# Performance work log

Measured on AMD Instinct MI355X. Metric: run time of the kernel, lower is better.

Reference implementation:

```python
import jax, jax.numpy as jnp
import numpy as np

D_MODEL = 256
N_HEADS = 4
D_HEAD = D_MODEL // N_HEADS
SCALE = 1.0 / np.sqrt(D_HEAD).astype(np.float32)


def setup_inputs() -> dict:
    key = jax.random.key(0)
    ks = jax.random.split(key, 8)
    B, T, S = 4, 512, 512
    return {
        "query": jax.random.normal(ks[0], (B, T, D_MODEL), dtype=jnp.float32),
        "key": jax.random.normal(ks[1], (B, S, D_MODEL), dtype=jnp.float32),
        "value": jax.random.normal(ks[2], (B, S, D_MODEL), dtype=jnp.float32),
        "w_q": jax.random.normal(ks[3], (D_MODEL, D_MODEL), dtype=jnp.float32) * 0.05,
        "w_k": jax.random.normal(ks[4], (D_MODEL, D_MODEL), dtype=jnp.float32) * 0.05,
        "w_v": jax.random.normal(ks[5], (D_MODEL, D_MODEL), dtype=jnp.float32) * 0.05,
        "v_a": jax.random.normal(ks[6], (N_HEADS, D_HEAD), dtype=jnp.float32),
        "w_o": jax.random.normal(ks[7], (D_MODEL, D_MODEL), dtype=jnp.float32) * 0.05,
    }


def reference(query, key, value, w_q, w_k, w_v, v_a, w_o):
    B, T, _ = query.shape
    S = key.shape[1]
    # projections; weights stored as (out, in) like nn.Linear -> x @ W.T
    Q = (query @ w_q.T).reshape(B, T, N_HEADS, D_HEAD).transpose(0, 2, 1, 3)  # bhtd
    K = (key @ w_k.T).reshape(B, S, N_HEADS, D_HEAD).transpose(0, 2, 1, 3)    # bhsd
    V = (value @ w_v.T).reshape(B, S, N_HEADS, D_HEAD).transpose(0, 2, 1, 3)  # bhsd
    # additive (Bahdanau) scores: tanh broadcast of shape (B,H,T,S,Dh)
    combined = jnp.tanh(Q[:, :, :, None, :] + K[:, :, None, :, :])
    scores = jnp.einsum('bhtsd,hd->bhts', combined, v_a) * SCALE
    attn = jax.nn.softmax(scores, axis=-1)  # (B,H,T,S)
    attended = jnp.einsum('bhts,bhsd->bhtd', attn, V)
    attended = attended.transpose(0, 2, 1, 3).reshape(B, T, D_MODEL)
    out = attended @ w_o.T
    return out, attn
```

## Files before the change

### kernel.cpp

```cpp
#include <hip/hip_runtime.h>
#include <math.h>

#define BATCH 4
#define TLEN 512
#define SLEN 512
#define DM 256
#define NH 4
#define DH 64
#define BT (BATCH * TLEN)

__device__ __forceinline__ float rcp_fast(float x) { return __builtin_amdgcn_rcpf(x); }

__global__ __launch_bounds__(256) void transposeN_kernel(
    const float* __restrict__ s0, const float* __restrict__ s1,
    const float* __restrict__ s2, const float* __restrict__ s3,
    float* __restrict__ d0, float* __restrict__ d1,
    float* __restrict__ d2, float* __restrict__ d3) {
  __shared__ float tile[64][65];
  int m = blockIdx.y;
  const float* S = (m == 0) ? s0 : (m == 1) ? s1 : (m == 2) ? s2 : s3;
  float* D = (m == 0) ? d0 : (m == 1) ? d1 : (m == 2) ? d2 : d3;
  int bx = blockIdx.x;
  int to = (bx & 3) * 64;
  int tk = (bx >> 2) * 64;
  int lo = threadIdx.x >> 6;
  int lk = threadIdx.x & 63;
#pragma unroll
  for (int p = 0; p < 16; ++p) {
    int o = p * 4 + lo;
    tile[o][lk] = S[(size_t)(to + o) * DM + tk + lk];
  }
  __syncthreads();
#pragma unroll
  for (int p = 0; p < 16; ++p) {
    int kk = p * 4 + lo;
    D[(size_t)(tk + kk) * DM + to + lk] = tile[lk][kk];
  }
}

__global__ __launch_bounds__(256) void proj_kernel(
    const float* __restrict__ q, const float* __restrict__ k, const float* __restrict__ v,
    const float* __restrict__ wqt, const float* __restrict__ wkt, const float* __restrict__ wvt,
    float* __restrict__ EQ, float* __restrict__ EKT, float* __restrict__ Vw) {
  int tid = threadIdx.x;
  int lane = tid & 63;
  int wid = __builtin_amdgcn_readfirstlane(tid >> 6);
  int which = blockIdx.y;
  const float* X = (which == 0) ? q : (which == 1) ? k : v;
  const float* WT = (which == 0) ? wqt : (which == 1) ? wkt : wvt;
  int row0 = (blockIdx.x >> 2) * 16 + wid * 4;
  int o = (blockIdx.x & 3) * 64 + lane;
  const float* xb = X + (size_t)row0 * DM;
  const float* wcol = WT + o;
  float a0 = 0.f, a1 = 0.f, a2 = 0.f, a3 = 0.f;
#pragma unroll 8
  for (int kk = 0; kk < DM; ++kk) {
    float w = wcol[(size_t)kk * DM];
    a0 = fmaf(xb[kk], w, a0);
    a1 = fmaf(xb[DM + kk], w, a1);
    a2 = fmaf(xb[2 * DM + kk], w, a2);
    a3 = fmaf(xb[3 * DM + kk], w, a3);
  }
  int h = o >> 6, d = o & 63;
  float accs[4] = {a0, a1, a2, a3};
#pragma unroll
  for (int r = 0; r < 4; ++r) {
    int row = row0 + r;
    int b = row >> 9, t = row & 511;
    int bh = b * NH + h;
    float val = accs[r];
    if (which < 2) {
      val = __expf(2.f * fminf(fmaxf(val, -5.5f), 5.5f));
    }
    if (which == 0) {
      EQ[((size_t)bh * TLEN + t) * DH + d] = val;
    } else if (which == 1) {
      EKT[(((size_t)bh * 16 + (d >> 2)) * SLEN + t) * 4 + (d & 3)] = val;
    } else {
      Vw[(size_t)bh * SLEN * DH + (size_t)(t >> 1) * 128 + d * 2 + (t & 1)] = val;
    }
  }
}

__global__ __launch_bounds__(256, 8) void attn_kernel(
    const float* __restrict__ EQ, const float* __restrict__ EKT,
    const float* __restrict__ Vw, const float* __restrict__ va_g,
    float* __restrict__ attn_out, float* __restrict__ attended) {
  __shared__ float pw[4][SLEN];
  __shared__ float fp[4][4][64];
  __shared__ float sred[4][4];
  int tid = threadIdx.x;
  int lane = tid & 63;
  int wid = __builtin_amdgcn_readfirstlane(tid >> 6);
  int bx = (int)((blockIdx.x & 7) * 256 + (blockIdx.x >> 3));
  int bh = bx >> 7;
  int tile = (bx & 127) * 4;
  int h = bh & 3, b = bh >> 2;
  int sq0 = wid * 128;

  const float4* ekf = (const float4*)EKT + (size_t)bh * (16 * SLEN) + sq0 + lane;
  const float* eqb = EQ + ((size_t)bh * TLEN + tile) * DH;
  const float* vap = va_g + h * DH;

  float acc[4][2];
#pragma unroll
  for (int t = 0; t < 4; ++t) { acc[t][0] = 0.f; acc[t][1] = 0.f; }
  float vsum = 0.f;

  float4 eA0, eA1, eB0, eB1;

#define LOADE(EV, dc_) do { EV##0 = ekf[(size_t)(dc_) * SLEN]; \
                            EV##1 = ekf[(size_t)(dc_) * SLEN + 64]; } while (0)

#define SC4(E, qv, av, aref) do {                                           \
    float A0 = fmaf(qv.x, E.x, 1.f), A1 = fmaf(qv.y, E.y, 1.f);             \
    float A2 = fmaf(qv.z, E.z, 1.f), A3 = fmaf(qv.w, E.w, 1.f);             \
    float n01 = fmaf(av.x, A1, av.y * A0);                                  \
    float n23 = fmaf(av.z, A3, av.w * A2);                                  \
    float P01 = A0 * A1, P23 = A2 * A3;                                     \
    float Nm = fmaf(n01, P23, n23 * P01);                                   \
    aref = fmaf(Nm, rcp_fast(P01 * P23), aref);                             \
  } while (0)

#define DCBODY(CUR, NXT, dc_) do {                                          \
    float4 av = *(const float4*)(vap + (dc_) * 4);                          \
    float4 q0 = *(const float4*)(eqb + 0 * DH + (dc_) * 4);                 \
    float4 q1 = *(const float4*)(eqb + 1 * DH + (dc_) * 4);                 \
    float4 q2 = *(const float4*)(eqb + 2 * DH + (dc_) * 4);                 \
    float4 q3 = *(const float4*)(eqb + 3 * DH + (dc_) * 4);                 \
    vsum += (av.x + av.y) + (av.z + av.w);                                  \
    if ((dc_) < 15) LOADE(NXT, (dc_) + 1);                                  \
    __builtin_amdgcn_sched_barrier(0);                                      \
    SC4(CUR##0, q0, av, acc[0][0]); SC4(CUR##1, q0, av, acc[0][1]);         \
    SC4(CUR##0, q1, av, acc[1][0]); SC4(CUR##1, q1, av, acc[1][1]);         \
    SC4(CUR##0, q2, av, acc[2][0]); SC4(CUR##1, q2, av, acc[2][1]);         \
    SC4(CUR##0, q3, av, acc[3][0]); SC4(CUR##1, q3, av, acc[3][1]);         \
  } while (0)

  LOADE(eA, 0);
#pragma unroll 1
  for (int dc2 = 0; dc2 < 8; ++dc2) {
    DCBODY(eA, eB, 2 * dc2);
    DCBODY(eB, eA, 2 * dc2 + 1);
  }

  size_t bht = (size_t)bh * TLEN + tile;
  float e0[4], e1[4];
#pragma unroll
  for (int t = 0; t < 4; ++t) {
    float x0 = __expf(fmaf(acc[t][0], -0.25f, vsum * 0.125f));
    float x1 = __expf(fmaf(acc[t][1], -0.25f, vsum * 0.125f));
    e0[t] = x0; e1[t] = x1;
    float es = x0 + x1;
#pragma unroll
    for (int off = 32; off; off >>= 1) es += __shfl_xor(es, off);
    if (lane == 0) sred[t][wid] = es;
  }
  __syncthreads();
#pragma unroll
  for (int t = 0; t < 4; ++t) {
    float es = (sred[t][0] + sred[t][1]) + (sred[t][2] + sred[t][3]);
    float inv = rcp_fast(es);
    float p0 = e0[t] * inv, p1 = e1[t] * inv;
    pw[t][sq0 + lane] = p0;
    pw[t][sq0 + 64 + lane] = p1;
    float* arow = attn_out + (bht + t) * SLEN + sq0;
    arow[lane] = p0;
    arow[64 + lane] = p1;
  }

  const float2* vb = (const float2*)Vw + (size_t)bh * (256 * 64) + (size_t)(wid * 64) * 64 + lane;
  float f[4];
#pragma unroll
  for (int t = 0; t < 4; ++t) f[t] = 0.f;
#pragma unroll 2
  for (int i = 0; i < 32; ++i) {
    float2 v01 = vb[(size_t)i * 128];
    float2 v23 = vb[(size_t)i * 128 + 64];
    int sb = sq0 + i * 4;
#pragma unroll
    for (int t = 0; t < 4; ++t) {
      float4 pq = *(const float4*)&pw[t][sb];
      f[t] = fmaf(pq.x, v01.x, f[t]);
      f[t] = fmaf(pq.y, v01.y, f[t]);
      f[t] = fmaf(pq.z, v23.x, f[t]);
      f[t] = fmaf(pq.w, v23.y, f[t]);
    }
  }
#pragma unroll
  for (int t = 0; t < 4; ++t) fp[wid][t][lane] = f[t];
  __syncthreads();
  {
    int t = wid;
    float s = (fp[0][t][lane] + fp[1][t][lane]) + (fp[2][t][lane] + fp[3][t][lane]);
    attended[((size_t)(b * TLEN) + tile + t) * DM + h * DH + lane] = s;
  }
}

__global__ __launch_bounds__(256) void outproj_kernel(
    const float* __restrict__ att, const float* __restrict__ wot,
    float* __restrict__ out) {
  int tid = threadIdx.x;
  int lane = tid & 63;
  int wid = __builtin_amdgcn_readfirstlane(tid >> 6);
  int row0 = (blockIdx.x >> 2) * 16 + wid * 4;
  int o = (blockIdx.x & 3) * 64 + lane;
  const float* xb = att + (size_t)row0 * DM;
  const float* wcol = wot + o;
  float a0 = 0.f, a1 = 0.f, a2 = 0.f, a3 = 0.f;
#pragma unroll 8
  for (int kk = 0; kk < DM; ++kk) {
    float w = wcol[(size_t)kk * DM];
    a0 = fmaf(xb[kk], w, a0);
    a1 = fmaf(xb[DM + kk], w, a1);
    a2 = fmaf(xb[2 * DM + kk], w, a2);
    a3 = fmaf(xb[3 * DM + kk], w, a3);
  }
  out[(size_t)(row0 + 0) * DM + o] = a0;
  out[(size_t)(row0 + 1) * DM + o] = a1;
  out[(size_t)(row0 + 2) * DM + o] = a2;
  out[(size_t)(row0 + 3) * DM + o] = a3;
}

extern "C" void kernel_launch(void* const* d_in, const int* in_sizes, int n_in,
                              void* d_out, int out_size, void* d_ws, size_t ws_size,
                              hipStream_t stream) {
  const float* query = (const float*)d_in[0];
  const float* key   = (const float*)d_in[1];
  const float* value = (const float*)d_in[2];
  const float* wq    = (const float*)d_in[3];
  const float* wk    = (const float*)d_in[4];
  const float* wv    = (const float*)d_in[5];
  const float* va    = (const float*)d_in[6];
  const float* wo    = (const float*)d_in[7];

  float* out  = (float*)d_out;
  float* attn = out + (size_t)BT * DM;

  const size_t SEG = (size_t)BT * DM;
  float* EQ  = (float*)d_ws;
  float* EKT = EQ + SEG;
  float* Vw  = EKT + SEG;
  float* att = Vw + SEG;

  bool big_ws = ws_size >= (4 * SEG + 4 * (size_t)DM * DM) * sizeof(float);

  if (big_ws) {
    float* WTq = att + SEG;
    float* WTk = WTq + (size_t)DM * DM;
    float* WTv = WTk + (size_t)DM * DM;
    float* WoT = WTv + (size_t)DM * DM;
    transposeN_kernel<<<dim3(16, 4), 256, 0, stream>>>(wq, wk, wv, wo, WTq, WTk, WTv, WoT);
    proj_kernel<<<dim3(512, 3), 256, 0, stream>>>(query, key, value, WTq, WTk, WTv, EQ, EKT, Vw);
    attn_kernel<<<dim3(2048), 256, 0, stream>>>(EQ, EKT, Vw, va, attn, att);
    outproj_kernel<<<dim3(512), 256, 0, stream>>>(att, WoT, out);
  } else {
    float* WTq = att;
    float* WTk = att + (size_t)DM * DM;
    float* WTv = att + 2 * (size_t)DM * DM;
    float* WoT = EQ;
    transposeN_kernel<<<dim3(16, 3), 256, 0, stream>>>(wq, wk, wv, wv, WTq, WTk, WTv, WTv);
    proj_kernel<<<dim3(512, 3), 256, 0, stream>>>(query, key, value, WTq, WTk, WTv, EQ, EKT, Vw);
    attn_kernel<<<dim3(2048), 256, 0, stream>>>(EQ, EKT, Vw, va, attn, att);
    transposeN_kernel<<<dim3(16, 1), 256, 0, stream>>>(wo, wo, wo, wo, WoT, WoT, WoT, WoT);
    outproj_kernel<<<dim3(512), 256, 0, stream>>>(att, WoT, out);
  }
}
```

Baseline: 88.71 us.

## Stage weight tiles in LDS and drop separate weight transpose kernel

Removes the transpose kernel launch. The projection and output-projection GEMMs now load untransposed weight rows into padded LDS in two K-halves, and each wave computes 8 rows instead of 4, which halves the grid. This saves one launch and the global transpose round-trip, and raises reuse of each weight value. The cost is extra syncthreads, about 33KB of LDS per block, and fewer blocks, which lowers occupancy and parallelism.

```diff
diff --git a/kernel.cpp b/kernel.cpp
--- a/kernel.cpp
+++ b/kernel.cpp
@@ -8,67 +8,69 @@
 #define NH 4
 #define DH 64
 #define BT (BATCH * TLEN)
+#define WPAD 132
 
 __device__ __forceinline__ float rcp_fast(float x) { return __builtin_amdgcn_rcpf(x); }
 
-__global__ __launch_bounds__(256) void transposeN_kernel(
-    const float* __restrict__ s0, const float* __restrict__ s1,
-    const float* __restrict__ s2, const float* __restrict__ s3,
-    float* __restrict__ d0, float* __restrict__ d1,
-    float* __restrict__ d2, float* __restrict__ d3) {
-  __shared__ float tile[64][65];
-  int m = blockIdx.y;
-  const float* S = (m == 0) ? s0 : (m == 1) ? s1 : (m == 2) ? s2 : s3;
-  float* D = (m == 0) ? d0 : (m == 1) ? d1 : (m == 2) ? d2 : d3;
-  int bx = blockIdx.x;
-  int to = (bx & 3) * 64;
-  int tk = (bx >> 2) * 64;
-  int lo = threadIdx.x >> 6;
-  int lk = threadIdx.x & 63;
-#pragma unroll
-  for (int p = 0; p < 16; ++p) {
-    int o = p * 4 + lo;
-    tile[o][lk] = S[(size_t)(to + o) * DM + tk + lk];
-  }
-  __syncthreads();
-#pragma unroll
-  for (int p = 0; p < 16; ++p) {
-    int kk = p * 4 + lo;
-    D[(size_t)(tk + kk) * DM + to + lk] = tile[lk][kk];
+__device__ __forceinline__ void gemm_selfstage(const float* __restrict__ X,
+                                               const float* __restrict__ W,
+                                               float* __restrict__ wlds,
+                                               int row0, int o0, int tid, int lane,
+                                               float* acc) {
+#pragma unroll
+  for (int r = 0; r < 8; ++r) acc[r] = 0.f;
+  const float* xb = X + (size_t)row0 * DM;
+#pragma unroll 1
+  for (int half = 0; half < 2; ++half) {
+    __syncthreads();
+    {
+      const float4* wsrc = (const float4*)(W + (size_t)o0 * DM + half * 128);
+#pragma unroll
+      for (int i = 0; i < 8; ++i) {
+        int c = i * 256 + tid;
+        int row = c >> 5, kq = c & 31;
+        *(float4*)&wlds[row * WPAD + kq * 4] = wsrc[(size_t)row * 64 + kq];
+      }
+    }
+    __syncthreads();
+    const float* xh = xb + half * 128;
+#pragma unroll 2
+    for (int kk = 0; kk < 128; kk += 4) {
+      float4 w = *(const float4*)&wlds[lane * WPAD + kk];
+#pragma unroll
+      for (int r = 0; r < 8; ++r) {
+        acc[r] = fmaf(xh[r * DM + kk + 0], w.x, acc[r]);
+        acc[r] = fmaf(xh[r * DM + kk + 1], w.y, acc[r]);
+        acc[r] = fmaf(xh[r * DM + kk + 2], w.z, acc[r]);
+        acc[r] = fmaf(xh[r * DM + kk + 3], w.w, acc[r]);
+      }
+    }
   }
 }
 
 __global__ __launch_bounds__(256) void proj_kernel(
     const float* __restrict__ q, const float* __restrict__ k, const float* __restrict__ v,
-    const float* __restrict__ wqt, const float* __restrict__ wkt, const float* __restrict__ wvt,
+    const float* __restrict__ wq, const float* __restrict__ wk, const float* __restrict__ wv,
     float* __restrict__ EQ, float* __restrict__ EKT, float* __restrict__ Vw) {
+  __shared__ float wlds[64 * WPAD];
   int tid = threadIdx.x;
   int lane = tid & 63;
   int wid = __builtin_amdgcn_readfirstlane(tid >> 6);
   int which = blockIdx.y;
   const float* X = (which == 0) ? q : (which == 1) ? k : v;
-  const float* WT = (which == 0) ? wqt : (which == 1) ? wkt : wvt;
-  int row0 = (blockIdx.x >> 2) * 16 + wid * 4;
-  int o = (blockIdx.x & 3) * 64 + lane;
-  const float* xb = X + (size_t)row0 * DM;
-  const float* wcol = WT + o;
-  float a0 = 0.f, a1 = 0.f, a2 = 0.f, a3 = 0.f;
-#pragma unroll 8
-  for (int kk = 0; kk < DM; ++kk) {
-    float w = wcol[(size_t)kk * DM];
-    a0 = fmaf(xb[kk], w, a0);
-    a1 = fmaf(xb[DM + kk], w, a1);
-    a2 = fmaf(xb[2 * DM + kk], w, a2);
-    a3 = fmaf(xb[3 * DM + kk], w, a3);
-  }
+  const float* W = (which == 0) ? wq : (which == 1) ? wk : wv;
+  int row0 = (blockIdx.x >> 2) * 32 + wid * 8;
+  int o0 = (blockIdx.x & 3) * 64;
+  float acc[8];
+  gemm_selfstage(X, W, wlds, row0, o0, tid, lane, acc);
+  int o = o0 + lane;
   int h = o >> 6, d = o & 63;
-  float accs[4] = {a0, a1, a2, a3};
-#pragma unroll
-  for (int r = 0; r < 4; ++r) {
+#pragma unroll
+  for (int r = 0; r < 8; ++r) {
     int row = row0 + r;
     int b = row >> 9, t = row & 511;
     int bh = b * NH + h;
-    float val = accs[r];
+    float val = acc[r];
     if (which < 2) {
       val = __expf(2.f * fminf(fmaxf(val, -5.5f), 5.5f));
     }
@@ -198,28 +200,20 @@
 }
 
 __global__ __launch_bounds__(256) void outproj_kernel(
-    const float* __restrict__ att, const float* __restrict__ wot,
+    const float* __restrict__ att, const float* __restrict__ wo,
     float* __restrict__ out) {
+  __shared__ float wlds[64 * WPAD];
   int tid = threadIdx.x;
   int lane = tid & 63;
   int wid = __builtin_amdgcn_readfirstlane(tid >> 6);
-  int row0 = (blockIdx.x >> 2) * 16 + wid * 4;
-  int o = (blockIdx.x & 3) * 64 + lane;
-  const float* xb = att + (size_t)row0 * DM;
-  const float* wcol = wot + o;
-  float a0 = 0.f, a1 = 0.f, a2 = 0.f, a3 = 0.f;
-#pragma unroll 8
-  for (int kk = 0; kk < DM; ++kk) {
-    float w = wcol[(size_t)kk * DM];
-    a0 = fmaf(xb[kk], w, a0);
-    a1 = fmaf(xb[DM + kk], w, a1);
-    a2 = fmaf(xb[2 * DM + kk], w, a2);
-    a3 = fmaf(xb[3 * DM + kk], w, a3);
-  }
-  out[(size_t)(row0 + 0) * DM + o] = a0;
-  out[(size_t)(row0 + 1) * DM + o] = a1;
-  out[(size_t)(row0 + 2) * DM + o] = a2;
-  out[(size_t)(row0 + 3) * DM + o] = a3;
+  int row0 = (blockIdx.x >> 2) * 32 + wid * 8;
+  int o0 = (blockIdx.x & 3) * 64;
+  float acc[8];
+  gemm_selfstage(att, wo, wlds, row0, o0, tid, lane, acc);
+  int o = o0 + lane;
+#pragma unroll
+  for (int r = 0; r < 8; ++r)
+    out[(size_t)(row0 + r) * DM + o] = acc[r];
 }
 
 extern "C" void kernel_launch(void* const* d_in, const int* in_sizes, int n_in,
@@ -243,26 +237,7 @@
   float* Vw  = EKT + SEG;
   float* att = Vw + SEG;
 
-  bool big_ws = ws_size >= (4 * SEG + 4 * (size_t)DM * DM) * sizeof(float);
-
-  if (big_ws) {
-    float* WTq = att + SEG;
-    float* WTk = WTq + (size_t)DM * DM;
-    float* WTv = WTk + (size_t)DM * DM;
-    float* WoT = WTv + (size_t)DM * DM;
-    transposeN_kernel<<<dim3(16, 4), 256, 0, stream>>>(wq, wk, wv, wo, WTq, WTk, WTv, WoT);
-    proj_kernel<<<dim3(512, 3), 256, 0, stream>>>(query, key, value, WTq, WTk, WTv, EQ, EKT, Vw);
-    attn_kernel<<<dim3(2048), 256, 0, stream>>>(EQ, EKT, Vw, va, attn, att);
-    outproj_kernel<<<dim3(512), 256, 0, stream>>>(att, WoT, out);
-  } else {
-    float* WTq = att;
-    float* WTk = att + (size_t)DM * DM;
-    float* WTv = att + 2 * (size_t)DM * DM;
-    float* WoT = EQ;
-    transposeN_kernel<<<dim3(16, 3), 256, 0, stream>>>(wq, wk, wv, wv, WTq, WTk, WTv, WTv);
-    proj_kernel<<<dim3(512, 3), 256, 0, stream>>>(query, key, value, WTq, WTk, WTv, EQ, EKT, Vw);
-    attn_kernel<<<dim3(2048), 256, 0, stream>>>(EQ, EKT, Vw, va, attn, att);
-    transposeN_kernel<<<dim3(16, 1), 256, 0, stream>>>(wo, wo, wo, wo, WoT, WoT, WoT, WoT);
-    outproj_kernel<<<dim3(512), 256, 0, stream>>>(att, WoT, out);
-  }
-}
+  proj_kernel<<<dim3(256, 3), 256, 0, stream>>>(query, key, value, wq, wk, wv, EQ, EKT, Vw);
+  attn_kernel<<<dim3(2048), 256, 0, stream>>>(EQ, EKT, Vw, va, attn, att);
+  outproj_kernel<<<dim3(256), 256, 0, stream>>>(att, wo, out);
+}
```

Result: slower. 101.8 us (+14.8%).
